# Kernel tuning notes

Hardware: AMD Instinct MI355X
Metric: run time of the kernel (lower is better)

The kernel has to match this reference:

```python
import jax, jax.numpy as jnp
import numpy as np

B, D, H, DEPTH = 1024, 1024, 1024, 4


def setup_inputs() -> dict:
    key = jax.random.key(0)
    k_x, k_w, k_ws, k_bs = jax.random.split(key, 4)
    x = jax.random.normal(k_x, (B, D), dtype=jnp.float32)
    W_enc = jax.random.normal(k_w, (D, H), dtype=jnp.float32) * 0.02
    b_enc = jnp.zeros((H,), dtype=jnp.float32)
    # per-layer CrossNet weights, matching keras random_normal init (stddev=0.05)
    ws = jax.random.normal(k_ws, (DEPTH, H, 1), dtype=jnp.float32) * 0.05
    bs = jax.random.normal(k_bs, (DEPTH, H, 1), dtype=jnp.float32) * 0.05
    return {"x": x, "W_enc": W_enc, "b_enc": b_enc, "ws": ws, "bs": bs}


def reference(x, W_enc, b_enc, ws, bs):
    # encoder Dense
    h = jnp.matmul(x, W_enc) + b_enc  # (B, H)
    x0 = h
    x_l = h
    depth = ws.shape[0]
    for l in range(depth):
        # original: (x0[:, :, None] * x_l[:, None, :]) @ w + b, squeezed.
        # outer[b,i,j] @ w  == x0[b,i] * sum_j x_l[b,j] * w[j]
        s = jnp.matmul(x_l, ws[l])            # (B, 1)
        residual = x0 * s + bs[l][:, 0]       # (B, H)
        x_l = residual + x_l
    return x_l
```

## Files before the change

kernel.cpp:

```cpp
#include <hip/hip_runtime.h>
#include <hip/hip_bf16.h>


#define B_SZ 1024
#define D_SZ 1024
#define H_SZ 1024
#define DEPTH 4

typedef _Float16 half4_t __attribute__((ext_vector_type(4)));
typedef _Float16 half8_t __attribute__((ext_vector_type(8)));
typedef float floatx4_t __attribute__((ext_vector_type(4)));

typedef const __attribute__((address_space(1))) unsigned int* gas_ptr;
typedef __attribute__((address_space(3))) unsigned int* las_ptr;

__device__ __forceinline__ void async_copy16(const void* g, void* l) {
    __builtin_amdgcn_global_load_lds((gas_ptr)g, (las_ptr)l, 16, 0, 0);
}

__global__ __launch_bounds__(256) void prep_kernel(
        const float* __restrict__ x, const float* __restrict__ W,
        _Float16* __restrict__ xh, _Float16* __restrict__ Wt) {
    const int b = blockIdx.x;
    const int t = threadIdx.x;
    if (b < 256) {
        __shared__ float S[64][65];
        const int k0 = (b >> 4) << 6;
        const int n0 = (b & 15) << 6;
#pragma unroll
        for (int i = 0; i < 4; ++i) {
            int idx = (i << 8) + t;
            int r = idx >> 4;
            int c4 = idx & 15;
            float4 v = *(const float4*)(W + (size_t)(k0 + r) * H_SZ + n0 + (c4 << 2));
            S[r][(c4 << 2) + 0] = v.x;
            S[r][(c4 << 2) + 1] = v.y;
            S[r][(c4 << 2) + 2] = v.z;
            S[r][(c4 << 2) + 3] = v.w;
        }
        __syncthreads();
#pragma unroll
        for (int i = 0; i < 4; ++i) {
            int idx = (i << 8) + t;
            int n = idx >> 4;
            int c4 = idx & 15;
            int k = c4 << 2;
            half4_t o;
            o.x = (_Float16)S[k + 0][n];
            o.y = (_Float16)S[k + 1][n];
            o.z = (_Float16)S[k + 2][n];
            o.w = (_Float16)S[k + 3][n];
            *(half4_t*)(Wt + (size_t)(n0 + n) * D_SZ + k0 + k) = o;
        }
    } else {
        const int base = (b - 256) * 4096;
#pragma unroll
        for (int i = 0; i < 4; ++i) {
            int off = base + (((i << 8) + t) << 2);
            float4 v = *(const float4*)(x + off);
            half4_t o;
            o.x = (_Float16)v.x; o.y = (_Float16)v.y;
            o.z = (_Float16)v.z; o.w = (_Float16)v.w;
            *(half4_t*)(xh + off) = o;
        }
    }
}

__global__ __launch_bounds__(512) void gemm_kernel(
        const _Float16* __restrict__ xh, const _Float16* __restrict__ Wt,
        float* __restrict__ h) {
    __shared__ _Float16 As[2][32 * 64];
    __shared__ _Float16 Bs[2][64 * 64];
    const int tid  = threadIdx.x;
    const int lane = tid & 63;
    const int w    = tid >> 6;
    const int m0 = blockIdx.y << 5;
    const int n0 = blockIdx.x << 6;
    const int wm = (w >> 2) << 4;
    const int wn = (w & 3) << 4;

    const int sr = tid >> 3;
    const int sc = ((tid & 7) ^ (sr & 7)) << 3;
    const _Float16* aSrc = xh + (size_t)(m0 + (sr & 31)) * D_SZ + sc;
    const _Float16* bSrc = Wt + (size_t)(n0 + sr) * D_SZ + sc;

    const int ra = wm + (lane & 15);
    const int rb = wn + (lane & 15);
    const int q  = lane >> 4;

    floatx4_t acc = {0.0f, 0.0f, 0.0f, 0.0f};

    if (tid < 256) async_copy16(aSrc, &As[0][tid << 3]);
    async_copy16(bSrc, &Bs[0][tid << 3]);

    for (int it = 0; it < 16; ++it) {
        __syncthreads();
        if (it + 1 < 16) {
            int k0 = (it + 1) << 6;
            int buf = (it + 1) & 1;
            if (tid < 256) async_copy16(aSrc + k0, &As[buf][tid << 3]);
            async_copy16(bSrc + k0, &Bs[buf][tid << 3]);
        }
        const _Float16* Ab = As[it & 1];
        const _Float16* Bb = Bs[it & 1];
#pragma unroll
        for (int kk = 0; kk < 2; ++kk) {
            int l = (kk << 2) + q;
            half8_t af = *(const half8_t*)(Ab + ra * 64 + ((l ^ (ra & 7)) << 3));
            half8_t bf = *(const half8_t*)(Bb + rb * 64 + ((l ^ (rb & 7)) << 3));
            acc = __builtin_amdgcn_mfma_f32_16x16x32_f16(af, bf, acc, 0, 0, 0);
        }
    }

    const int col = n0 + wn + (lane & 15);
    const int row0 = m0 + wm + (q << 2);
#pragma unroll
    for (int r = 0; r < 4; ++r)
        h[(size_t)(row0 + r) * H_SZ + col] = acc[r];
}

__global__ __launch_bounds__(256) void crossnet_kernel(
        float* __restrict__ h, const float* __restrict__ b_enc,
        const float* __restrict__ ws, const float* __restrict__ bs) {
    const int row = blockIdx.x;
    const int t = threadIdx.x;
    float* hr = h + (size_t)row * H_SZ;

    float4 hv = *(const float4*)(hr + (t << 2));
    float4 be = *(const float4*)(b_enc + (t << 2));
    float4 wv[DEPTH], bv[DEPTH];
#pragma unroll
    for (int l = 0; l < DEPTH; ++l) {
        wv[l] = *(const float4*)(ws + l * H_SZ + (t << 2));
        bv[l] = *(const float4*)(bs + l * H_SZ + (t << 2));
    }
    float x0[4] = {hv.x + be.x, hv.y + be.y, hv.z + be.z, hv.w + be.w};
    float xl[4] = {x0[0], x0[1], x0[2], x0[3]};

    __shared__ float red[DEPTH][4];

#pragma unroll
    for (int l = 0; l < DEPTH; ++l) {
        float p = xl[0] * wv[l].x + xl[1] * wv[l].y + xl[2] * wv[l].z + xl[3] * wv[l].w;
#pragma unroll
        for (int off = 32; off > 0; off >>= 1) p += __shfl_down(p, off, 64);
        if ((t & 63) == 0) red[l][t >> 6] = p;
        __syncthreads();
        float s = red[l][0] + red[l][1] + red[l][2] + red[l][3];
        xl[0] += x0[0] * s + bv[l].x;
        xl[1] += x0[1] * s + bv[l].y;
        xl[2] += x0[2] * s + bv[l].z;
        xl[3] += x0[3] * s + bv[l].w;
    }
    float4 o = {xl[0], xl[1], xl[2], xl[3]};
    *(float4*)(hr + (t << 2)) = o;
}

extern "C" void kernel_launch(void* const* d_in, const int* in_sizes, int n_in,
                              void* d_out, int out_size, void* d_ws, size_t ws_size,
                              hipStream_t stream) {
    const float* x     = (const float*)d_in[0];
    const float* W_enc = (const float*)d_in[1];
    const float* b_enc = (const float*)d_in[2];
    const float* ws    = (const float*)d_in[3];
    const float* bs    = (const float*)d_in[4];
    float* out = (float*)d_out;

    _Float16* xh = (_Float16*)d_ws;
    _Float16* Wt = xh + (size_t)B_SZ * D_SZ;

    prep_kernel<<<512, 256, 0, stream>>>(x, W_enc, xh, Wt);
    dim3 grid(H_SZ / 64, B_SZ / 32);
    gemm_kernel<<<grid, 512, 0, stream>>>(xh, Wt, out);
    crossnet_kernel<<<B_SZ, 256, 0, stream>>>(out, b_enc, ws, bs);
}
```

Baseline: 82.76 us.

## Fuse GEMM with CrossNet into one row-block kernel, convert x on the fly

```diff
diff --git a/kernel.cpp b/kernel.cpp
--- a/kernel.cpp
+++ b/kernel.cpp
@@ -11,149 +11,146 @@
 typedef _Float16 half8_t __attribute__((ext_vector_type(8)));
 typedef float floatx4_t __attribute__((ext_vector_type(4)));
 
-typedef const __attribute__((address_space(1))) unsigned int* gas_ptr;
-typedef __attribute__((address_space(3))) unsigned int* las_ptr;
-
-__device__ __forceinline__ void async_copy16(const void* g, void* l) {
-    __builtin_amdgcn_global_load_lds((gas_ptr)g, (las_ptr)l, 16, 0, 0);
+__global__ __launch_bounds__(256) void prep_kernel(
+        const float* __restrict__ W, _Float16* __restrict__ Wt) {
+    const int b = blockIdx.x;
+    const int t = threadIdx.x;
+    __shared__ float S[64][65];
+    const int k0 = (b >> 4) << 6;
+    const int n0 = (b & 15) << 6;
+#pragma unroll
+    for (int i = 0; i < 4; ++i) {
+        int idx = (i << 8) + t;
+        int r = idx >> 4;
+        int c4 = idx & 15;
+        float4 v = *(const float4*)(W + (size_t)(k0 + r) * H_SZ + n0 + (c4 << 2));
+        S[r][(c4 << 2) + 0] = v.x;
+        S[r][(c4 << 2) + 1] = v.y;
+        S[r][(c4 << 2) + 2] = v.z;
+        S[r][(c4 << 2) + 3] = v.w;
+    }
+    __syncthreads();
+#pragma unroll
+    for (int i = 0; i < 4; ++i) {
+        int idx = (i << 8) + t;
+        int n = idx >> 4;
+        int c4 = idx & 15;
+        int k = c4 << 2;
+        half4_t o;
+        o.x = (_Float16)S[k + 0][n];
+        o.y = (_Float16)S[k + 1][n];
+        o.z = (_Float16)S[k + 2][n];
+        o.w = (_Float16)S[k + 3][n];
+        *(half4_t*)(Wt + (size_t)(n0 + n) * D_SZ + k0 + k) = o;
+    }
 }
 
-__global__ __launch_bounds__(256) void prep_kernel(
-        const float* __restrict__ x, const float* __restrict__ W,
-        _Float16* __restrict__ xh, _Float16* __restrict__ Wt) {
-    const int b = blockIdx.x;
-    const int t = threadIdx.x;
-    if (b < 256) {
-        __shared__ float S[64][65];
-        const int k0 = (b >> 4) << 6;
-        const int n0 = (b & 15) << 6;
+__global__ __launch_bounds__(512, 2) void fused_kernel(
+        const float* __restrict__ x, const _Float16* __restrict__ Wt,
+        const float* __restrict__ b_enc, const float* __restrict__ ws,
+        const float* __restrict__ bs, float* __restrict__ out) {
+    __shared__ _Float16 Ash[16][1032];
+    __shared__ float red[DEPTH][16][8];
+
+    const int tid  = threadIdx.x;
+    const int lane = tid & 63;
+    const int w    = tid >> 6;
+    const int m0   = blockIdx.x << 4;
+
+    {
+        const int r  = tid >> 5;
+        const int cb = (tid & 31) << 2;
+        const float* src = x + (size_t)(m0 + r) * D_SZ;
 #pragma unroll
-        for (int i = 0; i < 4; ++i) {
-            int idx = (i << 8) + t;
-            int r = idx >> 4;
-            int c4 = idx & 15;
-            float4 v = *(const float4*)(W + (size_t)(k0 + r) * H_SZ + n0 + (c4 << 2));
-            S[r][(c4 << 2) + 0] = v.x;
-            S[r][(c4 << 2) + 1] = v.y;
-            S[r][(c4 << 2) + 2] = v.z;
-            S[r][(c4 << 2) + 3] = v.w;
-        }
-        __syncthreads();
-#pragma unroll
-        for (int i = 0; i < 4; ++i) {
-            int idx = (i << 8) + t;
-            int n = idx >> 4;
-            int c4 = idx & 15;
-            int k = c4 << 2;
-            half4_t o;
-            o.x = (_Float16)S[k + 0][n];
-            o.y = (_Float16)S[k + 1][n];
-            o.z = (_Float16)S[k + 2][n];
-            o.w = (_Float16)S[k + 3][n];
-            *(half4_t*)(Wt + (size_t)(n0 + n) * D_SZ + k0 + k) = o;
-        }
-    } else {
-        const int base = (b - 256) * 4096;
-#pragma unroll
-        for (int i = 0; i < 4; ++i) {
-            int off = base + (((i << 8) + t) << 2);
-            float4 v = *(const float4*)(x + off);
+        for (int i = 0; i < 8; ++i) {
+            int c = cb + (i << 7);
+            float4 v = *(const float4*)(src + c);
             half4_t o;
             o.x = (_Float16)v.x; o.y = (_Float16)v.y;
             o.z = (_Float16)v.z; o.w = (_Float16)v.w;
-            *(half4_t*)(xh + off) = o;
+            *(half4_t*)(&Ash[r][c]) = o;
         }
     }
-}
+    __syncthreads();
 
-__global__ __launch_bounds__(512) void gemm_kernel(
-        const _Float16* __restrict__ xh, const _Float16* __restrict__ Wt,
-        float* __restrict__ h) {
-    __shared__ _Float16 As[2][32 * 64];
-    __shared__ _Float16 Bs[2][64 * 64];
-    const int tid  = threadIdx.x;
-    const int lane = tid & 63;
-    const int w    = tid >> 6;
-    const int m0 = blockIdx.y << 5;
-    const int n0 = blockIdx.x << 6;
-    const int wm = (w >> 2) << 4;
-    const int wn = (w & 3) << 4;
+    const int cq = lane & 15;
+    const int q  = lane >> 4;
+    const _Float16* ap = &Ash[cq][q << 3];
+    const _Float16* bp = Wt + (size_t)((w << 7) + cq) * D_SZ + (q << 3);
 
-    const int sr = tid >> 3;
-    const int sc = ((tid & 7) ^ (sr & 7)) << 3;
-    const _Float16* aSrc = xh + (size_t)(m0 + (sr & 31)) * D_SZ + sc;
-    const _Float16* bSrc = Wt + (size_t)(n0 + sr) * D_SZ + sc;
+    floatx4_t acc[8];
+#pragma unroll
+    for (int t = 0; t < 8; ++t) acc[t] = (floatx4_t){0.f, 0.f, 0.f, 0.f};
 
-    const int ra = wm + (lane & 15);
-    const int rb = wn + (lane & 15);
-    const int q  = lane >> 4;
-
-    floatx4_t acc = {0.0f, 0.0f, 0.0f, 0.0f};
-
-    if (tid < 256) async_copy16(aSrc, &As[0][tid << 3]);
-    async_copy16(bSrc, &Bs[0][tid << 3]);
-
-    for (int it = 0; it < 16; ++it) {
-        __syncthreads();
-        if (it + 1 < 16) {
-            int k0 = (it + 1) << 6;
-            int buf = (it + 1) & 1;
-            if (tid < 256) async_copy16(aSrc + k0, &As[buf][tid << 3]);
-            async_copy16(bSrc + k0, &Bs[buf][tid << 3]);
-        }
-        const _Float16* Ab = As[it & 1];
-        const _Float16* Bb = Bs[it & 1];
+#pragma unroll 2
+    for (int kc = 0; kc < 32; ++kc) {
+        half8_t af = *(const half8_t*)(ap + (kc << 5));
 #pragma unroll
-        for (int kk = 0; kk < 2; ++kk) {
-            int l = (kk << 2) + q;
-            half8_t af = *(const half8_t*)(Ab + ra * 64 + ((l ^ (ra & 7)) << 3));
-            half8_t bf = *(const half8_t*)(Bb + rb * 64 + ((l ^ (rb & 7)) << 3));
-            acc = __builtin_amdgcn_mfma_f32_16x16x32_f16(af, bf, acc, 0, 0, 0);
+        for (int t = 0; t < 8; ++t) {
+            half8_t bf = *(const half8_t*)(bp + t * (16 * D_SZ) + (kc << 5));
+            acc[t] = __builtin_amdgcn_mfma_f32_16x16x32_f16(af, bf, acc[t], 0, 0, 0);
         }
     }
 
-    const int col = n0 + wn + (lane & 15);
-    const int row0 = m0 + wm + (q << 2);
+    float be[8], wv[DEPTH][8], bv[DEPTH][8];
 #pragma unroll
-    for (int r = 0; r < 4; ++r)
-        h[(size_t)(row0 + r) * H_SZ + col] = acc[r];
-}
+    for (int t = 0; t < 8; ++t) {
+        int col = (w << 7) + (t << 4) + cq;
+        be[t] = b_enc[col];
+#pragma unroll
+        for (int l = 0; l < DEPTH; ++l) {
+            wv[l][t] = ws[l * H_SZ + col];
+            bv[l][t] = bs[l * H_SZ + col];
+        }
+    }
+    float x0[8][4], xl[8][4];
+#pragma unroll
+    for (int t = 0; t < 8; ++t)
+#pragma unroll
+        for (int r = 0; r < 4; ++r) {
+            x0[t][r] = acc[t][r] + be[t];
+            xl[t][r] = x0[t][r];
+        }
 
-__global__ __launch_bounds__(256) void crossnet_kernel(
-        float* __restrict__ h, const float* __restrict__ b_enc,
-        const float* __restrict__ ws, const float* __restrict__ bs) {
-    const int row = blockIdx.x;
-    const int t = threadIdx.x;
-    float* hr = h + (size_t)row * H_SZ;
-
-    float4 hv = *(const float4*)(hr + (t << 2));
-    float4 be = *(const float4*)(b_enc + (t << 2));
-    float4 wv[DEPTH], bv[DEPTH];
+    const int r0 = q << 2;
 #pragma unroll
     for (int l = 0; l < DEPTH; ++l) {
-        wv[l] = *(const float4*)(ws + l * H_SZ + (t << 2));
-        bv[l] = *(const float4*)(bs + l * H_SZ + (t << 2));
+        float p[4];
+#pragma unroll
+        for (int r = 0; r < 4; ++r) {
+            p[r] = xl[0][r] * wv[l][0];
+#pragma unroll
+            for (int t = 1; t < 8; ++t) p[r] += xl[t][r] * wv[l][t];
+        }
+#pragma unroll
+        for (int off = 8; off > 0; off >>= 1)
+#pragma unroll
+            for (int r = 0; r < 4; ++r) p[r] += __shfl_down(p[r], off, 16);
+        if (cq == 0)
+#pragma unroll
+            for (int r = 0; r < 4; ++r) red[l][r0 + r][w] = p[r];
+        __syncthreads();
+        float s[4];
+#pragma unroll
+        for (int r = 0; r < 4; ++r) {
+            float4 a = *(const float4*)&red[l][r0 + r][0];
+            float4 b = *(const float4*)&red[l][r0 + r][4];
+            s[r] = (a.x + a.y) + (a.z + a.w) + (b.x + b.y) + (b.z + b.w);
+        }
+#pragma unroll
+        for (int t = 0; t < 8; ++t)
+#pragma unroll
+            for (int r = 0; r < 4; ++r)
+                xl[t][r] += x0[t][r] * s[r] + bv[l][t];
     }
-    float x0[4] = {hv.x + be.x, hv.y + be.y, hv.z + be.z, hv.w + be.w};
-    float xl[4] = {x0[0], x0[1], x0[2], x0[3]};
-
-    __shared__ float red[DEPTH][4];
 
 #pragma unroll
-    for (int l = 0; l < DEPTH; ++l) {
-        float p = xl[0] * wv[l].x + xl[1] * wv[l].y + xl[2] * wv[l].z + xl[3] * wv[l].w;
+    for (int t = 0; t < 8; ++t) {
+        int col = (w << 7) + (t << 4) + cq;
 #pragma unroll
-        for (int off = 32; off > 0; off >>= 1) p += __shfl_down(p, off, 64);
-        if ((t & 63) == 0) red[l][t >> 6] = p;
-        __syncthreads();
-        float s = red[l][0] + red[l][1] + red[l][2] + red[l][3];
-        xl[0] += x0[0] * s + bv[l].x;
-        xl[1] += x0[1] * s + bv[l].y;
-        xl[2] += x0[2] * s + bv[l].z;
-        xl[3] += x0[3] * s + bv[l].w;
+        for (int r = 0; r < 4; ++r)
+            out[(size_t)(m0 + r0 + r) * H_SZ + col] = xl[t][r];
     }
-    float4 o = {xl[0], xl[1], xl[2], xl[3]};
-    *(float4*)(hr + (t << 2)) = o;
 }
 
 extern "C" void kernel_launch(void* const* d_in, const int* in_sizes, int n_in,
@@ -166,11 +163,8 @@
     const float* bs    = (const float*)d_in[4];
     float* out = (float*)d_out;
 
-    _Float16* xh = (_Float16*)d_ws;
-    _Float16* Wt = xh + (size_t)B_SZ * D_SZ;
+    _Float16* Wt = (_Float16*)d_ws;
 
-    prep_kernel<<<512, 256, 0, stream>>>(x, W_enc, xh, Wt);
-    dim3 grid(H_SZ / 64, B_SZ / 32);
-    gemm_kernel<<<grid, 512, 0, stream>>>(xh, Wt, out);
-    crossnet_kernel<<<B_SZ, 256, 0, stream>>>(out, b_enc, ws, bs);
+    prep_kernel<<<256, 256, 0, stream>>>(W_enc, Wt);
+    fused_kernel<<<B_SZ / 16, 512, 0, stream>>>(x, Wt, b_enc, ws, bs, out);
 }
```

Measured after the change: 130.6 us. 1.58x slower.

## Fuse prep, GEMM and CrossNet into one cooperative kernel with grid syncs

Applied to the files above, without the earlier changes.

```diff
diff --git a/kernel.cpp b/kernel.cpp
--- a/kernel.cpp
+++ b/kernel.cpp
@@ -1,5 +1,8 @@
 #include <hip/hip_runtime.h>
+#include <hip/hip_cooperative_groups.h>
 #include <hip/hip_bf16.h>
+
+namespace cg = cooperative_groups;
 
 
 #define B_SZ 1024
@@ -18,13 +21,24 @@
     __builtin_amdgcn_global_load_lds((gas_ptr)g, (las_ptr)l, 16, 0, 0);
 }
 
-__global__ __launch_bounds__(256) void prep_kernel(
+union SharedU {
+    float S[64][65];
+    _Float16 G[2][6144];
+    float red[DEPTH][4];
+};
+
+__global__ __launch_bounds__(256, 4) void mono_kernel(
         const float* __restrict__ x, const float* __restrict__ W,
-        _Float16* __restrict__ xh, _Float16* __restrict__ Wt) {
+        const float* __restrict__ b_enc, const float* __restrict__ ws,
+        const float* __restrict__ bs, float* __restrict__ out,
+        _Float16* __restrict__ xh, _Float16* __restrict__ Wt,
+        float* __restrict__ h) {
+    __shared__ SharedU u;
     const int b = blockIdx.x;
     const int t = threadIdx.x;
+    cg::grid_group grid = cg::this_grid();
+
     if (b < 256) {
-        __shared__ float S[64][65];
         const int k0 = (b >> 4) << 6;
         const int n0 = (b & 15) << 6;
 #pragma unroll
@@ -33,10 +47,10 @@
             int r = idx >> 4;
             int c4 = idx & 15;
             float4 v = *(const float4*)(W + (size_t)(k0 + r) * H_SZ + n0 + (c4 << 2));
-            S[r][(c4 << 2) + 0] = v.x;
-            S[r][(c4 << 2) + 1] = v.y;
-            S[r][(c4 << 2) + 2] = v.z;
-            S[r][(c4 << 2) + 3] = v.w;
+            u.S[r][(c4 << 2) + 0] = v.x;
+            u.S[r][(c4 << 2) + 1] = v.y;
+            u.S[r][(c4 << 2) + 2] = v.z;
+            u.S[r][(c4 << 2) + 3] = v.w;
         }
         __syncthreads();
 #pragma unroll
@@ -46,10 +60,10 @@
             int c4 = idx & 15;
             int k = c4 << 2;
             half4_t o;
-            o.x = (_Float16)S[k + 0][n];
-            o.y = (_Float16)S[k + 1][n];
-            o.z = (_Float16)S[k + 2][n];
-            o.w = (_Float16)S[k + 3][n];
+            o.x = (_Float16)u.S[k + 0][n];
+            o.y = (_Float16)u.S[k + 1][n];
+            o.z = (_Float16)u.S[k + 2][n];
+            o.w = (_Float16)u.S[k + 3][n];
             *(half4_t*)(Wt + (size_t)(n0 + n) * D_SZ + k0 + k) = o;
         }
     } else {
@@ -64,96 +78,101 @@
             *(half4_t*)(xh + off) = o;
         }
     }
-}
+    __threadfence();
+    grid.sync();
 
-__global__ __launch_bounds__(512) void gemm_kernel(
-        const _Float16* __restrict__ xh, const _Float16* __restrict__ Wt,
-        float* __restrict__ h) {
-    __shared__ _Float16 As[2][32 * 64];
-    __shared__ _Float16 Bs[2][64 * 64];
-    const int tid  = threadIdx.x;
-    const int lane = tid & 63;
-    const int w    = tid >> 6;
-    const int m0 = blockIdx.y << 5;
-    const int n0 = blockIdx.x << 6;
-    const int wm = (w >> 2) << 4;
-    const int wn = (w & 3) << 4;
+    {
+        const int lane = t & 63;
+        const int w    = t >> 6;
+        const int m0 = (b >> 4) << 5;
+        const int n0 = (b & 15) << 6;
+        const int wm = (w >> 1) << 4;
+        const int wn = (w & 1) << 5;
 
-    const int sr = tid >> 3;
-    const int sc = ((tid & 7) ^ (sr & 7)) << 3;
-    const _Float16* aSrc = xh + (size_t)(m0 + (sr & 31)) * D_SZ + sc;
-    const _Float16* bSrc = Wt + (size_t)(n0 + sr) * D_SZ + sc;
+        const int sr = t >> 3;
+        const int sc = ((t & 7) ^ (sr & 7)) << 3;
+        const _Float16* aSrc  = xh + (size_t)(m0 + sr) * D_SZ + sc;
+        const _Float16* bSrc0 = Wt + (size_t)(n0 + sr) * D_SZ + sc;
+        const _Float16* bSrc1 = Wt + (size_t)(n0 + sr + 32) * D_SZ + sc;
 
-    const int ra = wm + (lane & 15);
-    const int rb = wn + (lane & 15);
-    const int q  = lane >> 4;
+        const int cq = lane & 15;
+        const int q  = lane >> 4;
+        const int ra  = wm + cq;
+        const int rb0 = wn + cq;
+        const int rb1 = wn + 16 + cq;
 
-    floatx4_t acc = {0.0f, 0.0f, 0.0f, 0.0f};
+        floatx4_t acc0 = {0.f, 0.f, 0.f, 0.f};
+        floatx4_t acc1 = {0.f, 0.f, 0.f, 0.f};
 
-    if (tid < 256) async_copy16(aSrc, &As[0][tid << 3]);
-    async_copy16(bSrc, &Bs[0][tid << 3]);
+        async_copy16(aSrc,  &u.G[0][(w << 9)]);
+        async_copy16(bSrc0, &u.G[0][2048 + (w << 9)]);
+        async_copy16(bSrc1, &u.G[0][4096 + (w << 9)]);
 
-    for (int it = 0; it < 16; ++it) {
-        __syncthreads();
-        if (it + 1 < 16) {
-            int k0 = (it + 1) << 6;
-            int buf = (it + 1) & 1;
-            if (tid < 256) async_copy16(aSrc + k0, &As[buf][tid << 3]);
-            async_copy16(bSrc + k0, &Bs[buf][tid << 3]);
+        for (int it = 0; it < 16; ++it) {
+            __syncthreads();
+            if (it + 1 < 16) {
+                const int k0 = (it + 1) << 6;
+                _Float16* Gb = u.G[(it + 1) & 1];
+                async_copy16(aSrc + k0,  Gb + (w << 9));
+                async_copy16(bSrc0 + k0, Gb + 2048 + (w << 9));
+                async_copy16(bSrc1 + k0, Gb + 4096 + (w << 9));
+            }
+            const _Float16* Gb = u.G[it & 1];
+#pragma unroll
+            for (int kc = 0; kc < 2; ++kc) {
+                const int lc = (kc << 2) + q;
+                half8_t af  = *(const half8_t*)(Gb + ra * 64 + ((lc ^ (ra & 7)) << 3));
+                half8_t bf0 = *(const half8_t*)(Gb + 2048 + rb0 * 64 + ((lc ^ (rb0 & 7)) << 3));
+                half8_t bf1 = *(const half8_t*)(Gb + 2048 + rb1 * 64 + ((lc ^ (rb1 & 7)) << 3));
+                acc0 = __builtin_amdgcn_mfma_f32_16x16x32_f16(af, bf0, acc0, 0, 0, 0);
+                acc1 = __builtin_amdgcn_mfma_f32_16x16x32_f16(af, bf1, acc1, 0, 0, 0);
+            }
         }
-        const _Float16* Ab = As[it & 1];
-        const _Float16* Bb = Bs[it & 1];
+
+        const int col0 = n0 + wn + cq;
+        const int col1 = col0 + 16;
+        const int row0 = m0 + wm + (q << 2);
 #pragma unroll
-        for (int kk = 0; kk < 2; ++kk) {
-            int l = (kk << 2) + q;
-            half8_t af = *(const half8_t*)(Ab + ra * 64 + ((l ^ (ra & 7)) << 3));
-            half8_t bf = *(const half8_t*)(Bb + rb * 64 + ((l ^ (rb & 7)) << 3));
-            acc = __builtin_amdgcn_mfma_f32_16x16x32_f16(af, bf, acc, 0, 0, 0);
+        for (int r = 0; r < 4; ++r) {
+            h[(size_t)(row0 + r) * H_SZ + col0] = acc0[r];
+            h[(size_t)(row0 + r) * H_SZ + col1] = acc1[r];
         }
     }
+    __threadfence();
+    grid.sync();
 
-    const int col = n0 + wn + (lane & 15);
-    const int row0 = m0 + wm + (q << 2);
+    {
+        float4 be = *(const float4*)(b_enc + (t << 2));
+        float4 wv[DEPTH], bv[DEPTH];
 #pragma unroll
-    for (int r = 0; r < 4; ++r)
-        h[(size_t)(row0 + r) * H_SZ + col] = acc[r];
-}
-
-__global__ __launch_bounds__(256) void crossnet_kernel(
-        float* __restrict__ h, const float* __restrict__ b_enc,
-        const float* __restrict__ ws, const float* __restrict__ bs) {
-    const int row = blockIdx.x;
-    const int t = threadIdx.x;
-    float* hr = h + (size_t)row * H_SZ;
-
-    float4 hv = *(const float4*)(hr + (t << 2));
-    float4 be = *(const float4*)(b_enc + (t << 2));
-    float4 wv[DEPTH], bv[DEPTH];
+        for (int l = 0; l < DEPTH; ++l) {
+            wv[l] = *(const float4*)(ws + l * H_SZ + (t << 2));
+            bv[l] = *(const float4*)(bs + l * H_SZ + (t << 2));
+        }
+        for (int rr = 0; rr < 2; ++rr) {
+            const int row = (b << 1) + rr;
+            const float* hr = h + (size_t)row * H_SZ;
+            float4 hv = *(const float4*)(hr + (t << 2));
+            float x0[4] = {hv.x + be.x, hv.y + be.y, hv.z + be.z, hv.w + be.w};
+            float xl[4] = {x0[0], x0[1], x0[2], x0[3]};
 #pragma unroll
-    for (int l = 0; l < DEPTH; ++l) {
-        wv[l] = *(const float4*)(ws + l * H_SZ + (t << 2));
-        bv[l] = *(const float4*)(bs + l * H_SZ + (t << 2));
+            for (int l = 0; l < DEPTH; ++l) {
+                float p = xl[0] * wv[l].x + xl[1] * wv[l].y
+                        + xl[2] * wv[l].z + xl[3] * wv[l].w;
+#pragma unroll
+                for (int off = 32; off > 0; off >>= 1) p += __shfl_down(p, off, 64);
+                if ((t & 63) == 0) u.red[l][t >> 6] = p;
+                __syncthreads();
+                float s = u.red[l][0] + u.red[l][1] + u.red[l][2] + u.red[l][3];
+                xl[0] += x0[0] * s + bv[l].x;
+                xl[1] += x0[1] * s + bv[l].y;
+                xl[2] += x0[2] * s + bv[l].z;
+                xl[3] += x0[3] * s + bv[l].w;
+            }
+            float4 o = {xl[0], xl[1], xl[2], xl[3]};
+            *(float4*)(out + (size_t)row * H_SZ + (t << 2)) = o;
+        }
     }
-    float x0[4] = {hv.x + be.x, hv.y + be.y, hv.z + be.z, hv.w + be.w};
-    float xl[4] = {x0[0], x0[1], x0[2], x0[3]};
-
-    __shared__ float red[DEPTH][4];
-
-#pragma unroll
-    for (int l = 0; l < DEPTH; ++l) {
-        float p = xl[0] * wv[l].x + xl[1] * wv[l].y + xl[2] * wv[l].z + xl[3] * wv[l].w;
-#pragma unroll
-        for (int off = 32; off > 0; off >>= 1) p += __shfl_down(p, off, 64);
-        if ((t & 63) == 0) red[l][t >> 6] = p;
-        __syncthreads();
-        float s = red[l][0] + red[l][1] + red[l][2] + red[l][3];
-        xl[0] += x0[0] * s + bv[l].x;
-        xl[1] += x0[1] * s + bv[l].y;
-        xl[2] += x0[2] * s + bv[l].z;
-        xl[3] += x0[3] * s + bv[l].w;
-    }
-    float4 o = {xl[0], xl[1], xl[2], xl[3]};
-    *(float4*)(hr + (t << 2)) = o;
 }
 
 extern "C" void kernel_launch(void* const* d_in, const int* in_sizes, int n_in,
@@ -167,10 +186,10 @@
     float* out = (float*)d_out;
 
     _Float16* xh = (_Float16*)d_ws;
-    _Float16* Wt = xh + (size_t)B_SZ * D_SZ;
+    _Float16* Wt = xh + (1 << 20);
+    float*    h  = (float*)((char*)d_ws + (4u << 20));
 
-    prep_kernel<<<512, 256, 0, stream>>>(x, W_enc, xh, Wt);
-    dim3 grid(H_SZ / 64, B_SZ / 32);
-    gemm_kernel<<<grid, 512, 0, stream>>>(xh, Wt, out);
-    crossnet_kernel<<<B_SZ, 256, 0, stream>>>(out, b_enc, ws, bs);
+    void* args[] = {&x, &W_enc, &b_enc, &ws, &bs, &out, &xh, &Wt, &h};
+    hipLaunchCooperativeKernel((const void*)mono_kernel, dim3(512), dim3(256),
+                               args, 0, stream);
 }
```

New measurement: 314.0 us. 279% more time.
